# Kernel optimization log

Hardware: AMD Instinct MI355X
Metric: run time of the kernel (lower is better)

Reference implementation:

```python
import jax, jax.numpy as jnp
import numpy as np

B = 256          # batch
H = 1024         # conditioning_size (dec_hid_dim)
D = 256          # gst_dim
G = 32           # num_gst
C = 16           # num_cells
O = 256          # output_size


def setup_inputs() -> dict:
    key = jax.random.key(0)
    ks = jax.random.split(key, 7)
    hidden = jax.random.normal(ks[0], (B, H), dtype=jnp.float32)
    # per-cell embedding tables: nn.Embedding(num_gst, gst_dim) stacked over cells
    gst_emb = jax.random.normal(ks[1], (C, G, D), dtype=jnp.float32)
    # per-cell Linear(gst_dim + cond, cond): weight [H, H + D] (torch [out, in]), bias [H]
    attn_w = jax.random.normal(ks[2], (C, H, H + D), dtype=jnp.float32) * 0.02
    attn_b = jax.random.normal(ks[3], (C, H), dtype=jnp.float32) * 0.02
    # per-cell v: Parameter(torch.rand(cond))
    v = jax.random.uniform(ks[4], (C, H), dtype=jnp.float32)
    # out Linear(gst_dim, output_size)
    out_w = jax.random.normal(ks[5], (O, D), dtype=jnp.float32) * 0.02
    out_b = jax.random.normal(ks[6], (O,), dtype=jnp.float32) * 0.02
    return {"hidden": hidden, "gst_emb": gst_emb, "attn_w": attn_w,
            "attn_b": attn_b, "v": v, "out_w": out_w, "out_b": out_b}


def reference(hidden, gst_emb, attn_w, attn_b, v, out_w, out_b):
    # Original concatenates (hidden, encoder_outputs) along features; split the
    # linear weight accordingly instead of materializing the concat.
    w_hid = attn_w[:, :, :H]        # [C, H, H]
    w_enc = attn_w[:, :, H:]        # [C, H, D]
    # embedding lookup of arange(G) == the table rows themselves (same for all batch)
    enc = gst_emb                   # [C, G, D]
    hid_part = jnp.einsum('bh,coh->bco', hidden, w_hid)     # [B, C, Ho]
    enc_part = jnp.einsum('cgd,cod->cgo', enc, w_enc)       # [C, G, Ho]
    energy = jnp.tanh(hid_part[:, :, None, :] + enc_part[None]
                      + attn_b[None, :, None, :])           # [B, C, G, Ho]
    scores = jnp.einsum('bcgh,ch->bcg', energy, v)          # [B, C, G]
    attention = jax.nn.softmax(scores, axis=-1)             # softmax over num_gst
    weighted = jnp.einsum('bcg,cgd->bcd', attention, enc)   # [B, C, D]
    att_cat = attention.reshape(B, C * G)                   # torch.cat(att_list, dim=1)
    pooled = jnp.mean(weighted, axis=1)                     # [B, D]
    out = pooled @ out_w.T + out_b                          # [B, O]
    return (att_cat, out)
```

## Files before the change

kernel.cpp:

```cpp
#include <hip/hip_runtime.h>
#include <hip/hip_bf16.h>

#define B_  256
#define H_  1024
#define D_  256
#define G_  32
#define C_  16
#define O_  256
#define HD_ 1280
#define N1_ 16384
#define RS_ 36

typedef __attribute__((ext_vector_type(8))) short short8;
typedef __attribute__((ext_vector_type(4))) short s16x4;
typedef __attribute__((ext_vector_type(4))) float f32x4;

#define MFMA16(a, b, c) __builtin_amdgcn_mfma_f32_16x16x32_bf16((a), (b), (c), 0, 0, 0)

__device__ __forceinline__ float tanh_c(float x) {
    float y = __expf(2.f * x);
    float t = 1.f - 2.f * __builtin_amdgcn_rcpf(y + 1.f);
    return fminf(fmaxf(t, -0.99999994f), 0.99999994f);
}

__device__ __forceinline__ short bfhi(float x) {
    return (short)(__float_as_uint(x) >> 16);
}
__device__ __forceinline__ short bflo(float x) {
    float fhi = __uint_as_float(__float_as_uint(x) & 0xFFFF0000u);
    return (short)(__float_as_uint(x - fhi) >> 16);
}

__device__ __forceinline__ void split4(const float4 v, s16x4& hi, s16x4& lo) {
    hi[0] = bfhi(v.x); lo[0] = bflo(v.x);
    hi[1] = bfhi(v.y); lo[1] = bflo(v.y);
    hi[2] = bfhi(v.z); lo[2] = bflo(v.z);
    hi[3] = bfhi(v.w); lo[3] = bflo(v.w);
}

__global__ __launch_bounds__(512) void gemm1_kernel(
    const float* __restrict__ hidden, const float* __restrict__ attn_w,
    const float* __restrict__ attn_b, float* __restrict__ hp)
{
    __shared__ short AsH[128 * RS_];
    __shared__ short AsL[128 * RS_];
    __shared__ short BsH[64 * RS_];
    __shared__ short BsL[64 * RS_];

    const int tid  = threadIdx.x;
    const int wave = tid >> 6, lane = tid & 63;
    const int m0 = blockIdx.x * 128;
    const int n0 = blockIdx.y * 64;
    const int wm = (wave >> 1) * 32;
    const int wn = (wave & 1) * 32;
    const int l16 = lane & 15;
    const int lk  = (lane >> 4) * 8;

    f32x4 acc[2][2];
    for (int mi = 0; mi < 2; ++mi)
        for (int ni = 0; ni < 2; ++ni)
            acc[mi][ni] = f32x4{0.f, 0.f, 0.f, 0.f};

    int rA[2], cA[2];
    #pragma unroll
    for (int i = 0; i < 2; ++i) {
        const int chunk = tid + i * 512;
        rA[i] = chunk >> 3;
        cA[i] = (chunk & 7) * 4;
    }
    const int rB = tid >> 3, cB = (tid & 7) * 4;

    const float* pA0 = hidden + rA[0] * H_ + m0 * H_ + cA[0];
    const float* pA1 = hidden + rA[1] * H_ + m0 * H_ + cA[1];
    const float* pB  = attn_w + (size_t)(n0 + rB) * HD_ + cB;

    float4 va[2], vb;
    va[0] = *(const float4*)(pA0);
    va[1] = *(const float4*)(pA1);
    vb    = *(const float4*)(pB);

    for (int k0 = 0; k0 < H_; k0 += 32) {
        __syncthreads();
        #pragma unroll
        for (int i = 0; i < 2; ++i) {
            s16x4 h, l;
            split4(va[i], h, l);
            *(s16x4*)(AsH + rA[i] * RS_ + cA[i]) = h;
            *(s16x4*)(AsL + rA[i] * RS_ + cA[i]) = l;
        }
        {
            s16x4 h, l;
            split4(vb, h, l);
            *(s16x4*)(BsH + rB * RS_ + cB) = h;
            *(s16x4*)(BsL + rB * RS_ + cB) = l;
        }
        __syncthreads();

        if (k0 + 32 < H_) {
            const int kn = k0 + 32;
            va[0] = *(const float4*)(pA0 + kn);
            va[1] = *(const float4*)(pA1 + kn);
            vb    = *(const float4*)(pB  + kn);
        }

        short8 ah[2], al[2], bh[2], bl[2];
        #pragma unroll
        for (int mi = 0; mi < 2; ++mi) {
            ah[mi] = *(const short8*)(AsH + (wm + mi * 16 + l16) * RS_ + lk);
            al[mi] = *(const short8*)(AsL + (wm + mi * 16 + l16) * RS_ + lk);
        }
        #pragma unroll
        for (int ni = 0; ni < 2; ++ni) {
            bh[ni] = *(const short8*)(BsH + (wn + ni * 16 + l16) * RS_ + lk);
            bl[ni] = *(const short8*)(BsL + (wn + ni * 16 + l16) * RS_ + lk);
        }
        #pragma unroll
        for (int mi = 0; mi < 2; ++mi)
            #pragma unroll
            for (int ni = 0; ni < 2; ++ni) {
                acc[mi][ni] = MFMA16(ah[mi], bh[ni], acc[mi][ni]);
                acc[mi][ni] = MFMA16(al[mi], bh[ni], acc[mi][ni]);
                acc[mi][ni] = MFMA16(ah[mi], bl[ni], acc[mi][ni]);
            }
    }

    const int lr = (lane >> 4) * 4;
    #pragma unroll
    for (int mi = 0; mi < 2; ++mi) {
        #pragma unroll
        for (int ni = 0; ni < 2; ++ni) {
            const int col  = n0 + wn + ni * 16 + l16;
            const float bias = attn_b[col];
            float* dst = hp + (size_t)(m0 + wm + mi * 16 + lr) * N1_ + col;
            f32x4 vacc = acc[mi][ni];
            dst[0]        = tanh_c(vacc[0] + bias);
            dst[N1_]      = tanh_c(vacc[1] + bias);
            dst[2 * N1_]  = tanh_c(vacc[2] + bias);
            dst[3 * N1_]  = tanh_c(vacc[3] + bias);
        }
    }
}

__global__ __launch_bounds__(256) void gemm2_kernel(
    const float* __restrict__ enc, const float* __restrict__ attn_w,
    float* __restrict__ ep)
{
    const int tid  = threadIdx.x;
    const int wave = tid >> 6, lane = tid & 63;
    const int c  = blockIdx.y;
    const int n0 = blockIdx.x * 64 + wave * 16;
    const int l16 = lane & 15;
    const int lk  = (lane >> 4) * 8;

    f32x4 acc[2];
    acc[0] = f32x4{0.f, 0.f, 0.f, 0.f};
    acc[1] = f32x4{0.f, 0.f, 0.f, 0.f};

    const float* encp = enc + c * (G_ * D_);
    const float* wp   = attn_w + (size_t)c * H_ * HD_ + H_;

    #pragma unroll
    for (int kk = 0; kk < 8; ++kk) {
        const int k0 = kk * 32 + lk;
        short8 ah[2], al[2], bh, bl;
        #pragma unroll
        for (int mi = 0; mi < 2; ++mi) {
            const float* p = encp + (mi * 16 + l16) * D_ + k0;
            s16x4 h0, l0, h1, l1;
            split4(*(const float4*)p, h0, l0);
            split4(*(const float4*)(p + 4), h1, l1);
            ah[mi] = short8{h0[0],h0[1],h0[2],h0[3],h1[0],h1[1],h1[2],h1[3]};
            al[mi] = short8{l0[0],l0[1],l0[2],l0[3],l1[0],l1[1],l1[2],l1[3]};
        }
        {
            const float* p = wp + (size_t)(n0 + l16) * HD_ + k0;
            s16x4 h0, l0, h1, l1;
            split4(*(const float4*)p, h0, l0);
            split4(*(const float4*)(p + 4), h1, l1);
            bh = short8{h0[0],h0[1],h0[2],h0[3],h1[0],h1[1],h1[2],h1[3]};
            bl = short8{l0[0],l0[1],l0[2],l0[3],l1[0],l1[1],l1[2],l1[3]};
        }
        #pragma unroll
        for (int mi = 0; mi < 2; ++mi) {
            acc[mi] = MFMA16(ah[mi], bh, acc[mi]);
            acc[mi] = MFMA16(al[mi], bh, acc[mi]);
            acc[mi] = MFMA16(ah[mi], bl, acc[mi]);
        }
    }

    const int lr = (lane >> 4) * 4;
    #pragma unroll
    for (int mi = 0; mi < 2; ++mi) {
        const int g = mi * 16 + lr;
        const int o = n0 + l16;
        float* dst = ep + (c * G_ + g) * H_ + o;
        f32x4 vacc = acc[mi];
        dst[0]      = tanh_c(vacc[0]);
        dst[H_]     = tanh_c(vacc[1]);
        dst[2 * H_] = tanh_c(vacc[2]);
        dst[3 * H_] = tanh_c(vacc[3]);
    }
}

__global__ __launch_bounds__(256) void attn_kernel(
    const float* __restrict__ hp, const float* __restrict__ ep,
    const float* __restrict__ v, const float* __restrict__ enc,
    float* __restrict__ out, float* __restrict__ wt)
{
    const int c = blockIdx.x, b = blockIdx.y;
    const int tid  = threadIdx.x;
    const int wave = tid >> 6, lane = tid & 63;

    __shared__ float s_att[G_];
    __shared__ float s_sc[G_];

    float tav[16], vv[16];
    const float* hprow = hp + (size_t)b * N1_ + c * H_;
    const float* vrow  = v + c * H_;
    #pragma unroll
    for (int j = 0; j < 16; ++j) {
        const int o = lane + j * 64;
        tav[j] = hprow[o];
        vv[j]  = vrow[o];
    }

    #pragma unroll
    for (int gg = 0; gg < 8; ++gg) {
        const int g = wave * 8 + gg;
        const float* eprow = ep + (c * G_ + g) * H_;
        float s = 0.f;
        #pragma unroll
        for (int j = 0; j < 16; ++j) {
            const float tb  = eprow[lane + j * 64];
            const float ta  = tav[j];
            const float num = ta + tb;
            const float den = fmaf(ta, tb, 1.f);
            const float t   = num * __builtin_amdgcn_rcpf(den);
            s = fmaf(t, vv[j], s);
        }
        #pragma unroll
        for (int off = 32; off > 0; off >>= 1)
            s += __shfl_down(s, off, 64);
        if (lane == 0) s_sc[g] = s;
    }
    __syncthreads();

    if (tid < 32) {
        float s = s_sc[tid];
        float m = s;
        #pragma unroll
        for (int off = 16; off > 0; off >>= 1)
            m = fmaxf(m, __shfl_xor(m, off, 32));
        const float e = __expf(s - m);
        float sum = e;
        #pragma unroll
        for (int off = 16; off > 0; off >>= 1)
            sum += __shfl_xor(sum, off, 32);
        const float a = e / sum;
        s_att[tid] = a;
        out[(size_t)b * (C_ * G_) + c * G_ + tid] = a;
    }
    __syncthreads();

    float wsum = 0.f;
    const float* encc = enc + c * (G_ * D_) + tid;
    #pragma unroll
    for (int g = 0; g < G_; ++g)
        wsum += s_att[g] * encc[g * D_];
    wt[(size_t)(b * C_ + c) * D_ + tid] = wsum;
}

__global__ __launch_bounds__(256) void out_kernel(
    const float* __restrict__ wt, const float* __restrict__ out_w,
    const float* __restrict__ out_b, float* __restrict__ out)
{
    const int b = blockIdx.x, tid = threadIdx.x;
    __shared__ float pooled[D_];

    float s = 0.f;
    #pragma unroll
    for (int c = 0; c < C_; ++c)
        s += wt[(size_t)(b * C_ + c) * D_ + tid];
    pooled[tid] = s * (1.f / 16.f);
    __syncthreads();

    float acc = out_b[tid];
    const float* wrow = out_w + tid * D_;
    #pragma unroll 8
    for (int dc = 0; dc < 64; ++dc) {
        float4 w4 = *(const float4*)(wrow + dc * 4);
        acc += pooled[dc * 4 + 0] * w4.x;
        acc += pooled[dc * 4 + 1] * w4.y;
        acc += pooled[dc * 4 + 2] * w4.z;
        acc += pooled[dc * 4 + 3] * w4.w;
    }
    out[(size_t)B_ * (C_ * G_) + b * O_ + tid] = acc;
}

extern "C" void kernel_launch(void* const* d_in, const int* in_sizes, int n_in,
                              void* d_out, int out_size, void* d_ws, size_t ws_size,
                              hipStream_t stream) {
    const float* hidden = (const float*)d_in[0];
    const float* enc    = (const float*)d_in[1];
    const float* attn_w = (const float*)d_in[2];
    const float* attn_b = (const float*)d_in[3];
    const float* v      = (const float*)d_in[4];
    const float* out_w  = (const float*)d_in[5];
    const float* out_b  = (const float*)d_in[6];
    float* out = (float*)d_out;

    float* hp = (float*)d_ws;
    float* ep = hp + (size_t)B_ * N1_;
    float* wt = ep + (size_t)C_ * G_ * H_;

    gemm1_kernel<<<dim3(2, 256), 512, 0, stream>>>(hidden, attn_w, attn_b, hp);
    gemm2_kernel<<<dim3(16, C_), 256, 0, stream>>>(enc, attn_w, ep);
    attn_kernel<<<dim3(C_, B_), 256, 0, stream>>>(hp, ep, v, enc, out, wt);
    out_kernel<<<B_, 256, 0, stream>>>(wt, out_w, out_b, out);
}
```

Measured before the change: 206.5 us.

## Fuse hidden and encoder GEMMs into one launch, batch attention over four rows

```diff
diff --git a/kernel.cpp b/kernel.cpp
--- a/kernel.cpp
+++ b/kernel.cpp
@@ -38,167 +38,168 @@
     hi[3] = bfhi(v.w); lo[3] = bflo(v.w);
 }
 
-__global__ __launch_bounds__(512) void gemm1_kernel(
-    const float* __restrict__ hidden, const float* __restrict__ attn_w,
-    const float* __restrict__ attn_b, float* __restrict__ hp)
+__global__ __launch_bounds__(256) void gemm12_kernel(
+    const float* __restrict__ hidden, const float* __restrict__ enc,
+    const float* __restrict__ attn_w, const float* __restrict__ attn_b,
+    float* __restrict__ hp, float* __restrict__ ep)
 {
-    __shared__ short AsH[128 * RS_];
-    __shared__ short AsL[128 * RS_];
+    __shared__ short AsH[64 * RS_];
+    __shared__ short AsL[64 * RS_];
     __shared__ short BsH[64 * RS_];
     __shared__ short BsL[64 * RS_];
 
     const int tid  = threadIdx.x;
     const int wave = tid >> 6, lane = tid & 63;
-    const int m0 = blockIdx.x * 128;
-    const int n0 = blockIdx.y * 64;
-    const int wm = (wave >> 1) * 32;
-    const int wn = (wave & 1) * 32;
     const int l16 = lane & 15;
     const int lk  = (lane >> 4) * 8;
 
-    f32x4 acc[2][2];
-    for (int mi = 0; mi < 2; ++mi)
-        for (int ni = 0; ni < 2; ++ni)
-            acc[mi][ni] = f32x4{0.f, 0.f, 0.f, 0.f};
-
-    int rA[2], cA[2];
-    #pragma unroll
-    for (int i = 0; i < 2; ++i) {
-        const int chunk = tid + i * 512;
-        rA[i] = chunk >> 3;
-        cA[i] = (chunk & 7) * 4;
-    }
-    const int rB = tid >> 3, cB = (tid & 7) * 4;
-
-    const float* pA0 = hidden + rA[0] * H_ + m0 * H_ + cA[0];
-    const float* pA1 = hidden + rA[1] * H_ + m0 * H_ + cA[1];
-    const float* pB  = attn_w + (size_t)(n0 + rB) * HD_ + cB;
-
-    float4 va[2], vb;
-    va[0] = *(const float4*)(pA0);
-    va[1] = *(const float4*)(pA1);
-    vb    = *(const float4*)(pB);
-
-    for (int k0 = 0; k0 < H_; k0 += 32) {
-        __syncthreads();
-        #pragma unroll
-        for (int i = 0; i < 2; ++i) {
-            s16x4 h, l;
-            split4(va[i], h, l);
-            *(s16x4*)(AsH + rA[i] * RS_ + cA[i]) = h;
-            *(s16x4*)(AsL + rA[i] * RS_ + cA[i]) = l;
-        }
-        {
-            s16x4 h, l;
-            split4(vb, h, l);
-            *(s16x4*)(BsH + rB * RS_ + cB) = h;
-            *(s16x4*)(BsL + rB * RS_ + cB) = l;
-        }
-        __syncthreads();
-
-        if (k0 + 32 < H_) {
-            const int kn = k0 + 32;
-            va[0] = *(const float4*)(pA0 + kn);
-            va[1] = *(const float4*)(pA1 + kn);
-            vb    = *(const float4*)(pB  + kn);
-        }
-
-        short8 ah[2], al[2], bh[2], bl[2];
+    if (blockIdx.x < 4) {
+        const int m0 = blockIdx.x * 64;
+        const int n0 = blockIdx.y * 64;
+        const int wm = (wave >> 1) * 32;
+        const int wn = (wave & 1) * 32;
+
+        f32x4 acc[2][2];
+        #pragma unroll
+        for (int mi = 0; mi < 2; ++mi)
+            #pragma unroll
+            for (int ni = 0; ni < 2; ++ni)
+                acc[mi][ni] = f32x4{0.f, 0.f, 0.f, 0.f};
+
+        const int r0 = tid >> 3;
+        const int c0 = (tid & 7) * 4;
+        const float* pA = hidden + (size_t)(m0 + r0) * H_ + c0;
+        const float* pB = attn_w + (size_t)(n0 + r0) * HD_ + c0;
+        const int dA = 32 * H_;
+        const int dB = 32 * HD_;
+
+        float4 a0[2], a1[2], b0[2], b1[2];
+        a0[0] = *(const float4*)(pA);
+        a1[0] = *(const float4*)(pA + dA);
+        b0[0] = *(const float4*)(pB);
+        b1[0] = *(const float4*)(pB + dB);
+        a0[1] = *(const float4*)(pA + 32);
+        a1[1] = *(const float4*)(pA + dA + 32);
+        b0[1] = *(const float4*)(pB + 32);
+        b1[1] = *(const float4*)(pB + dB + 32);
+
+#define G1_BODY(S, K0)                                                        \
+        {                                                                     \
+            __builtin_amdgcn_s_barrier();                                     \
+            { s16x4 h_, l_; split4(a0[S], h_, l_);                            \
+              *(s16x4*)(AsH + r0 * RS_ + c0) = h_;                            \
+              *(s16x4*)(AsL + r0 * RS_ + c0) = l_; }                          \
+            { s16x4 h_, l_; split4(a1[S], h_, l_);                            \
+              *(s16x4*)(AsH + (r0 + 32) * RS_ + c0) = h_;                     \
+              *(s16x4*)(AsL + (r0 + 32) * RS_ + c0) = l_; }                   \
+            { s16x4 h_, l_; split4(b0[S], h_, l_);                            \
+              *(s16x4*)(BsH + r0 * RS_ + c0) = h_;                            \
+              *(s16x4*)(BsL + r0 * RS_ + c0) = l_; }                          \
+            { s16x4 h_, l_; split4(b1[S], h_, l_);                            \
+              *(s16x4*)(BsH + (r0 + 32) * RS_ + c0) = h_;                     \
+              *(s16x4*)(BsL + (r0 + 32) * RS_ + c0) = l_; }                   \
+            asm volatile("s_waitcnt lgkmcnt(0)" ::: "memory");                \
+            __builtin_amdgcn_s_barrier();                                     \
+            if ((K0) + 64 < H_) {                                             \
+                a0[S] = *(const float4*)(pA + (K0) + 64);                     \
+                a1[S] = *(const float4*)(pA + dA + (K0) + 64);                \
+                b0[S] = *(const float4*)(pB + (K0) + 64);                     \
+                b1[S] = *(const float4*)(pB + dB + (K0) + 64);                \
+            }                                                                 \
+            short8 ah_[2], al_[2], bh_[2], bl_[2];                            \
+            _Pragma("unroll")                                                 \
+            for (int mi = 0; mi < 2; ++mi) {                                  \
+                ah_[mi] = *(const short8*)(AsH + (wm + mi * 16 + l16) * RS_ + lk); \
+                al_[mi] = *(const short8*)(AsL + (wm + mi * 16 + l16) * RS_ + lk); \
+            }                                                                 \
+            _Pragma("unroll")                                                 \
+            for (int ni = 0; ni < 2; ++ni) {                                  \
+                bh_[ni] = *(const short8*)(BsH + (wn + ni * 16 + l16) * RS_ + lk); \
+                bl_[ni] = *(const short8*)(BsL + (wn + ni * 16 + l16) * RS_ + lk); \
+            }                                                                 \
+            _Pragma("unroll")                                                 \
+            for (int mi = 0; mi < 2; ++mi)                                    \
+                _Pragma("unroll")                                             \
+                for (int ni = 0; ni < 2; ++ni) {                              \
+                    acc[mi][ni] = MFMA16(ah_[mi], bh_[ni], acc[mi][ni]);      \
+                    acc[mi][ni] = MFMA16(al_[mi], bh_[ni], acc[mi][ni]);      \
+                    acc[mi][ni] = MFMA16(ah_[mi], bl_[ni], acc[mi][ni]);      \
+                }                                                             \
+        }
+
+        for (int k0 = 0; k0 < H_; k0 += 64) {
+            G1_BODY(0, k0)
+            G1_BODY(1, k0 + 32)
+        }
+#undef G1_BODY
+
+        const int lr = (lane >> 4) * 4;
         #pragma unroll
         for (int mi = 0; mi < 2; ++mi) {
-            ah[mi] = *(const short8*)(AsH + (wm + mi * 16 + l16) * RS_ + lk);
-            al[mi] = *(const short8*)(AsL + (wm + mi * 16 + l16) * RS_ + lk);
-        }
-        #pragma unroll
-        for (int ni = 0; ni < 2; ++ni) {
-            bh[ni] = *(const short8*)(BsH + (wn + ni * 16 + l16) * RS_ + lk);
-            bl[ni] = *(const short8*)(BsL + (wn + ni * 16 + l16) * RS_ + lk);
-        }
-        #pragma unroll
-        for (int mi = 0; mi < 2; ++mi)
             #pragma unroll
             for (int ni = 0; ni < 2; ++ni) {
-                acc[mi][ni] = MFMA16(ah[mi], bh[ni], acc[mi][ni]);
-                acc[mi][ni] = MFMA16(al[mi], bh[ni], acc[mi][ni]);
-                acc[mi][ni] = MFMA16(ah[mi], bl[ni], acc[mi][ni]);
-            }
-    }
-
-    const int lr = (lane >> 4) * 4;
-    #pragma unroll
-    for (int mi = 0; mi < 2; ++mi) {
-        #pragma unroll
-        for (int ni = 0; ni < 2; ++ni) {
-            const int col  = n0 + wn + ni * 16 + l16;
-            const float bias = attn_b[col];
-            float* dst = hp + (size_t)(m0 + wm + mi * 16 + lr) * N1_ + col;
-            f32x4 vacc = acc[mi][ni];
-            dst[0]        = tanh_c(vacc[0] + bias);
-            dst[N1_]      = tanh_c(vacc[1] + bias);
-            dst[2 * N1_]  = tanh_c(vacc[2] + bias);
-            dst[3 * N1_]  = tanh_c(vacc[3] + bias);
-        }
-    }
-}
-
-__global__ __launch_bounds__(256) void gemm2_kernel(
-    const float* __restrict__ enc, const float* __restrict__ attn_w,
-    float* __restrict__ ep)
-{
-    const int tid  = threadIdx.x;
-    const int wave = tid >> 6, lane = tid & 63;
-    const int c  = blockIdx.y;
-    const int n0 = blockIdx.x * 64 + wave * 16;
-    const int l16 = lane & 15;
-    const int lk  = (lane >> 4) * 8;
-
-    f32x4 acc[2];
-    acc[0] = f32x4{0.f, 0.f, 0.f, 0.f};
-    acc[1] = f32x4{0.f, 0.f, 0.f, 0.f};
-
-    const float* encp = enc + c * (G_ * D_);
-    const float* wp   = attn_w + (size_t)c * H_ * HD_ + H_;
-
-    #pragma unroll
-    for (int kk = 0; kk < 8; ++kk) {
-        const int k0 = kk * 32 + lk;
-        short8 ah[2], al[2], bh, bl;
+                const int col   = n0 + wn + ni * 16 + l16;
+                const float bias = attn_b[col];
+                float* dst = hp + (size_t)(m0 + wm + mi * 16 + lr) * N1_ + col;
+                f32x4 vacc = acc[mi][ni];
+                dst[0]       = tanh_c(vacc[0] + bias);
+                dst[N1_]     = tanh_c(vacc[1] + bias);
+                dst[2 * N1_] = tanh_c(vacc[2] + bias);
+                dst[3 * N1_] = tanh_c(vacc[3] + bias);
+            }
+        }
+    } else {
+        const int c  = blockIdx.y & 15;
+        const int n0 = (blockIdx.y >> 4) * 64 + wave * 16;
+
+        f32x4 acc[2];
+        acc[0] = f32x4{0.f, 0.f, 0.f, 0.f};
+        acc[1] = f32x4{0.f, 0.f, 0.f, 0.f};
+
+        const float* encp = enc + c * (G_ * D_);
+        const float* wp   = attn_w + (size_t)c * H_ * HD_ + H_;
+
+        #pragma unroll
+        for (int kk = 0; kk < 8; ++kk) {
+            const int k0 = kk * 32 + lk;
+            short8 ah[2], al[2], bh, bl;
+            #pragma unroll
+            for (int mi = 0; mi < 2; ++mi) {
+                const float* p = encp + (mi * 16 + l16) * D_ + k0;
+                s16x4 h0, l0, h1, l1;
+                split4(*(const float4*)p, h0, l0);
+                split4(*(const float4*)(p + 4), h1, l1);
+                ah[mi] = short8{h0[0],h0[1],h0[2],h0[3],h1[0],h1[1],h1[2],h1[3]};
+                al[mi] = short8{l0[0],l0[1],l0[2],l0[3],l1[0],l1[1],l1[2],l1[3]};
+            }
+            {
+                const float* p = wp + (size_t)(n0 + l16) * HD_ + k0;
+                s16x4 h0, l0, h1, l1;
+                split4(*(const float4*)p, h0, l0);
+                split4(*(const float4*)(p + 4), h1, l1);
+                bh = short8{h0[0],h0[1],h0[2],h0[3],h1[0],h1[1],h1[2],h1[3]};
+                bl = short8{l0[0],l0[1],l0[2],l0[3],l1[0],l1[1],l1[2],l1[3]};
+            }
+            #pragma unroll
+            for (int mi = 0; mi < 2; ++mi) {
+                acc[mi] = MFMA16(ah[mi], bh, acc[mi]);
+                acc[mi] = MFMA16(al[mi], bh, acc[mi]);
+                acc[mi] = MFMA16(ah[mi], bl, acc[mi]);
+            }
+        }
+
+        const int lr = (lane >> 4) * 4;
         #pragma unroll
         for (int mi = 0; mi < 2; ++mi) {
-            const float* p = encp + (mi * 16 + l16) * D_ + k0;
-            s16x4 h0, l0, h1, l1;
-            split4(*(const float4*)p, h0, l0);
-            split4(*(const float4*)(p + 4), h1, l1);
-            ah[mi] = short8{h0[0],h0[1],h0[2],h0[3],h1[0],h1[1],h1[2],h1[3]};
-            al[mi] = short8{l0[0],l0[1],l0[2],l0[3],l1[0],l1[1],l1[2],l1[3]};
-        }
-        {
-            const float* p = wp + (size_t)(n0 + l16) * HD_ + k0;
-            s16x4 h0, l0, h1, l1;
-            split4(*(const float4*)p, h0, l0);
-            split4(*(const float4*)(p + 4), h1, l1);
-            bh = short8{h0[0],h0[1],h0[2],h0[3],h1[0],h1[1],h1[2],h1[3]};
-            bl = short8{l0[0],l0[1],l0[2],l0[3],l1[0],l1[1],l1[2],l1[3]};
-        }
-        #pragma unroll
-        for (int mi = 0; mi < 2; ++mi) {
-            acc[mi] = MFMA16(ah[mi], bh, acc[mi]);
-            acc[mi] = MFMA16(al[mi], bh, acc[mi]);
-            acc[mi] = MFMA16(ah[mi], bl, acc[mi]);
-        }
-    }
-
-    const int lr = (lane >> 4) * 4;
-    #pragma unroll
-    for (int mi = 0; mi < 2; ++mi) {
-        const int g = mi * 16 + lr;
-        const int o = n0 + l16;
-        float* dst = ep + (c * G_ + g) * H_ + o;
-        f32x4 vacc = acc[mi];
-        dst[0]      = tanh_c(vacc[0]);
-        dst[H_]     = tanh_c(vacc[1]);
-        dst[2 * H_] = tanh_c(vacc[2]);
-        dst[3 * H_] = tanh_c(vacc[3]);
+            const int g = mi * 16 + lr;
+            const int o = n0 + l16;
+            float* dst = ep + (c * G_ + g) * H_ + o;
+            f32x4 vacc = acc[mi];
+            dst[0]      = tanh_c(vacc[0]);
+            dst[H_]     = tanh_c(vacc[1]);
+            dst[2 * H_] = tanh_c(vacc[2]);
+            dst[3 * H_] = tanh_c(vacc[3]);
+        }
     }
 }
 
@@ -207,67 +208,94 @@
     const float* __restrict__ v, const float* __restrict__ enc,
     float* __restrict__ out, float* __restrict__ wt)
 {
-    const int c = blockIdx.x, b = blockIdx.y;
+    const int c  = blockIdx.x;
+    const int b0 = blockIdx.y * 4;
     const int tid  = threadIdx.x;
     const int wave = tid >> 6, lane = tid & 63;
 
-    __shared__ float s_att[G_];
-    __shared__ float s_sc[G_];
-
-    float tav[16], vv[16];
-    const float* hprow = hp + (size_t)b * N1_ + c * H_;
-    const float* vrow  = v + c * H_;
-    #pragma unroll
-    for (int j = 0; j < 16; ++j) {
-        const int o = lane + j * 64;
-        tav[j] = hprow[o];
-        vv[j]  = vrow[o];
+    __shared__ float s_att[4][G_];
+    __shared__ float s_sc[4][G_];
+
+    f32x4 vv[4], tav[4][4];
+    const float* vrow = v + c * H_;
+    #pragma unroll
+    for (int j = 0; j < 4; ++j)
+        vv[j] = *(const f32x4*)(vrow + lane * 4 + j * 256);
+    #pragma unroll
+    for (int bi = 0; bi < 4; ++bi) {
+        const float* hprow = hp + (size_t)(b0 + bi) * N1_ + c * H_;
+        #pragma unroll
+        for (int j = 0; j < 4; ++j)
+            tav[bi][j] = *(const f32x4*)(hprow + lane * 4 + j * 256);
     }
 
     #pragma unroll
     for (int gg = 0; gg < 8; ++gg) {
         const int g = wave * 8 + gg;
-        const float* eprow = ep + (c * G_ + g) * H_;
-        float s = 0.f;
-        #pragma unroll
-        for (int j = 0; j < 16; ++j) {
-            const float tb  = eprow[lane + j * 64];
-            const float ta  = tav[j];
-            const float num = ta + tb;
-            const float den = fmaf(ta, tb, 1.f);
-            const float t   = num * __builtin_amdgcn_rcpf(den);
-            s = fmaf(t, vv[j], s);
-        }
-        #pragma unroll
-        for (int off = 32; off > 0; off >>= 1)
-            s += __shfl_down(s, off, 64);
-        if (lane == 0) s_sc[g] = s;
+        const float* eprow = ep + (size_t)(c * G_ + g) * H_;
+        float s[4] = {0.f, 0.f, 0.f, 0.f};
+        #pragma unroll
+        for (int j = 0; j < 4; ++j) {
+            const f32x4 tb = *(const f32x4*)(eprow + lane * 4 + j * 256);
+            #pragma unroll
+            for (int e = 0; e < 4; ++e) {
+                const float tbx = tb[e];
+                const float w   = vv[j][e];
+                #pragma unroll
+                for (int bi = 0; bi < 4; ++bi) {
+                    const float ta  = tav[bi][j][e];
+                    const float num = ta + tbx;
+                    const float den = fmaf(ta, tbx, 1.f);
+                    s[bi] = fmaf(num * __builtin_amdgcn_rcpf(den), w, s[bi]);
+                }
+            }
+        }
+        #pragma unroll
+        for (int off = 32; off > 0; off >>= 1) {
+            s[0] += __shfl_down(s[0], off, 64);
+            s[1] += __shfl_down(s[1], off, 64);
+            s[2] += __shfl_down(s[2], off, 64);
+            s[3] += __shfl_down(s[3], off, 64);
+        }
+        if (lane == 0) {
+            s_sc[0][g] = s[0]; s_sc[1][g] = s[1];
+            s_sc[2][g] = s[2]; s_sc[3][g] = s[3];
+        }
     }
     __syncthreads();
 
-    if (tid < 32) {
-        float s = s_sc[tid];
-        float m = s;
+    if (tid < 128) {
+        const int bi = tid >> 5, g = tid & 31;
+        float sv = s_sc[bi][g];
+        float m = sv;
         #pragma unroll
         for (int off = 16; off > 0; off >>= 1)
             m = fmaxf(m, __shfl_xor(m, off, 32));
-        const float e = __expf(s - m);
+        const float e = __expf(sv - m);
         float sum = e;
         #pragma unroll
         for (int off = 16; off > 0; off >>= 1)
             sum += __shfl_xor(sum, off, 32);
         const float a = e / sum;
-        s_att[tid] = a;
-        out[(size_t)b * (C_ * G_) + c * G_ + tid] = a;
+        s_att[bi][g] = a;
+        out[(size_t)(b0 + bi) * (C_ * G_) + c * G_ + g] = a;
     }
     __syncthreads();
 
-    float wsum = 0.f;
+    float w0 = 0.f, w1 = 0.f, w2 = 0.f, w3 = 0.f;
     const float* encc = enc + c * (G_ * D_) + tid;
     #pragma unroll
-    for (int g = 0; g < G_; ++g)
-        wsum += s_att[g] * encc[g * D_];
-    wt[(size_t)(b * C_ + c) * D_ + tid] = wsum;
+    for (int g = 0; g < G_; ++g) {
+        const float e = encc[g * D_];
+        w0 = fmaf(s_att[0][g], e, w0);
+        w1 = fmaf(s_att[1][g], e, w1);
+        w2 = fmaf(s_att[2][g], e, w2);
+        w3 = fmaf(s_att[3][g], e, w3);
+    }
+    wt[(size_t)((b0 + 0) * C_ + c) * D_ + tid] = w0;
+    wt[(size_t)((b0 + 1) * C_ + c) * D_ + tid] = w1;
+    wt[(size_t)((b0 + 2) * C_ + c) * D_ + tid] = w2;
+    wt[(size_t)((b0 + 3) * C_ + c) * D_ + tid] = w3;
 }
 
 __global__ __launch_bounds__(256) void out_kernel(
@@ -313,8 +341,7 @@
     float* ep = hp + (size_t)B_ * N1_;
     float* wt = ep + (size_t)C_ * G_ * H_;
 
-    gemm1_kernel<<<dim3(2, 256), 512, 0, stream>>>(hidden, attn_w, attn_b, hp);
-    gemm2_kernel<<<dim3(16, C_), 256, 0, stream>>>(enc, attn_w, ep);
-    attn_kernel<<<dim3(C_, B_), 256, 0, stream>>>(hp, ep, v, enc, out, wt);
+    gemm12_kernel<<<dim3(5, 256), 256, 0, stream>>>(hidden, enc, attn_w, attn_b, hp, ep);
+    attn_kernel<<<dim3(C_, B_ / 4), 256, 0, stream>>>(hp, ep, v, enc, out, wt);
     out_kernel<<<B_, 256, 0, stream>>>(wt, out_w, out_b, out);
 }
```

Result: slower. 220.4 us (+6.7%).
